# Kernel optimization log

Hardware: AMD Instinct MI355X
Metric: run time of the kernel (lower is better)

Reference implementation:

```python
import jax, jax.numpy as jnp
import numpy as np

B, L, D = 8, 1024, 768          # batch, seq_len, d_model
DI, DS, NL, DC = 1536, 16, 2, 4  # d_inner=2*d_model, d_state, n_layers, d_conv
DECAY, INSCALE = 0.9, 0.1
LN_EPS = 1e-5


def setup_inputs() -> dict:
    key = jax.random.key(0)
    ks = jax.random.split(key, 8)
    return {
        "x": jax.random.normal(ks[0], (B, L, D), jnp.float32),
        "in_proj_w": jax.random.normal(ks[1], (NL, D, 2 * DI), jnp.float32) * 0.02,
        "conv_w": jax.random.normal(ks[2], (NL, DI, DC), jnp.float32) * 0.1,
        "conv_b": jnp.zeros((NL, DI), jnp.float32),
        "out_proj_w": jax.random.normal(ks[3], (NL, DI, D), jnp.float32) * 0.02,
        "ln_gamma": jnp.ones((D,), jnp.float32),
        "ln_beta": jnp.zeros((D,), jnp.float32),
        # per-layer, per-timestep random state matrices (torch.randn inside the scan loop)
        "A": jax.random.normal(ks[4], (NL, L, DI, DS), jnp.float32),
        "Bm": jax.random.normal(ks[5], (NL, L, DS, DI), jnp.float32),
    }


def _silu(v):
    return v * jax.nn.sigmoid(v)


def _causal_dwconv(x, w, b):
    # x: [B, L, DI], w: [DI, DC], b: [DI]; torch Conv1d(groups=DI, padding=DC-1)[..., :L]
    xp = jnp.pad(x, ((0, 0), (DC - 1, 0), (0, 0)))
    out = b
    for k in range(DC):  # tiny fixed kernel loop
        out = out + w[:, k] * xp[:, k:k + L, :]
    return out


def _mamba_block(x, Wi, cw, cb, Wo, A_l, B_l):
    xz = jnp.einsum('bld,de->ble', x, Wi)
    x_in, z = jnp.split(xz, 2, axis=-1)          # each [B, L, DI]
    xc = _silu(_causal_dwconv(x_in, cw, cb))
    # selective scan: h_t = 0.9*h_{t-1} + 0.1 * x_t @ A_t ; y_t = h_t @ B_t
    u = INSCALE * jnp.einsum('blc,lcs->bls', xc, A_l)   # [B, L, DS]
    def step(h, u_t):
        h = DECAY * h + u_t
        return h, h
    _, hs = jax.lax.scan(step, jnp.zeros((x.shape[0], DS), x.dtype),
                         jnp.swapaxes(u, 0, 1))          # hs: [L, B, DS]
    x_ssm = jnp.einsum('lbs,lsc->blc', hs, B_l)          # [B, L, DI]
    y = x_ssm * _silu(z)
    return jnp.einsum('blc,cd->bld', y, Wo)


def reference(x, in_proj_w, conv_w, conv_b, out_proj_w, ln_gamma, ln_beta, A, Bm):
    for i in range(NL):  # residual fallback path of MambaSSM
        x = x + _mamba_block(x, in_proj_w[i], conv_w[i], conv_b[i],
                             out_proj_w[i], A[i], Bm[i])
    mu = jnp.mean(x, axis=-1, keepdims=True)
    var = jnp.mean(jnp.square(x - mu), axis=-1, keepdims=True)
    return (x - mu) / jnp.sqrt(var + LN_EPS) * ln_gamma + ln_beta
```

## Files before the change

### kernel.cpp

```cpp
#include <hip/hip_runtime.h>
#include <cstddef>
#include <cstdint>

constexpr int B  = 8;
constexpr int L  = 1024;
constexpr int D  = 768;
constexpr int DI = 1536;
constexpr int DS = 16;
constexpr int NL = 2;
constexpr float DECAY   = 0.9f;
constexpr float INSCALE = 0.1f;
constexpr float LN_EPS  = 1e-5f;

typedef __attribute__((ext_vector_type(8))) short bf16x8;
typedef __attribute__((ext_vector_type(4))) float f32x4;

typedef __attribute__((address_space(3))) uint32_t       lds_u32;
typedef const __attribute__((address_space(1))) uint32_t glb_u32;

__device__ __forceinline__ float siluf(float v) { return v / (1.0f + expf(-v)); }

__device__ __forceinline__ short f2bf(float f) {
  uint32_t u = __float_as_uint(f);
  u += 0x7fff + ((u >> 16) & 1);
  return (short)(u >> 16);
}
__device__ __forceinline__ float bf2f(short s) {
  return __uint_as_float(((uint32_t)(uint16_t)s) << 16);
}

__device__ __forceinline__ void load_lds16(const short* g, short* l) {
  __builtin_amdgcn_global_load_lds((glb_u32*)g, (lds_u32*)l, 16, 0, 0);
}

__global__ __launch_bounds__(256) void prep_kernel(const float* __restrict__ x,
                                                   short* __restrict__ xb,
                                                   const float* __restrict__ Wi,
                                                   const float* __restrict__ Wo,
                                                   short* __restrict__ Wt_i,
                                                   short* __restrict__ Wt_o) {
  int bid = blockIdx.x;
  if (bid < 6144) {
    int i = bid * 256 + threadIdx.x;
    float4 v = ((const float4*)x)[i];
    short4 s;
    s.x = f2bf(v.x); s.y = f2bf(v.y); s.z = f2bf(v.z); s.w = f2bf(v.w);
    ((short4*)xb)[i] = s;
    return;
  }
  bid -= 6144;
  __shared__ float t[32][33];
  const int layer = bid / 3456;
  bid %= 3456;
  const float* W; short* Wt; int K, N, bx, by;
  if (bid < 2304) {
    W  = Wi  + (size_t)layer * D * 2 * DI;
    Wt = Wt_i + (size_t)layer * 2 * DI * D;
    K = D; N = 2 * DI; bx = bid % 96; by = bid / 96;
  } else {
    bid -= 2304;
    W  = Wo  + (size_t)layer * DI * D;
    Wt = Wt_o + (size_t)layer * D * DI;
    K = DI; N = D; bx = bid % 24; by = bid / 24;
  }
  const int n0 = bx * 32, k0 = by * 32;
  const int tx = threadIdx.x & 31, ty = threadIdx.x >> 5;
#pragma unroll
  for (int r = ty; r < 32; r += 8) t[r][tx] = W[(size_t)(k0 + r) * N + n0 + tx];
  __syncthreads();
#pragma unroll
  for (int r = ty; r < 32; r += 8) Wt[(size_t)(n0 + r) * K + k0 + tx] = f2bf(t[tx][r]);
}

__global__ __launch_bounds__(256) void gemm_bt0(const short* __restrict__ A,
                                                const short* __restrict__ Bt,
                                                short* __restrict__ Pb,
                                                int M, int N, int K) {
  __shared__ short As[3][128 * 32];
  __shared__ short Bs[3][128 * 32];
  const int tid  = threadIdx.x;
  const int lane = tid & 63;
  const int w    = tid >> 6;
  const int wm   = w >> 1;
  const int wn   = w & 1;
  const int bm   = blockIdx.y * 128;
  const int bn   = blockIdx.x * 128;

  const int seg0 = w * 2;
  const int lane16 = lane << 4;
  const int P0 = (seg0 << 10) + lane16;
  const int Q0 = P0 ^ (((P0 >> 7) & 3) << 4);
  const int row0 = Q0 >> 6;
  const int g0   = (Q0 >> 4) & 3;
  const int P1 = ((seg0 + 1) << 10) + lane16;
  const int Q1 = P1 ^ (((P1 >> 7) & 3) << 4);
  const int row1 = Q1 >> 6;
  const int g1   = (Q1 >> 4) & 3;

  const short* gA0 = A  + (size_t)(bm + row0) * K + g0 * 8;
  const short* gA1 = A  + (size_t)(bm + row1) * K + g1 * 8;
  const short* gB0 = Bt + (size_t)(bn + row0) * K + g0 * 8;
  const short* gB1 = Bt + (size_t)(bn + row1) * K + g1 * 8;

  f32x4 acc[4][4];
#pragma unroll
  for (int i = 0; i < 4; ++i)
#pragma unroll
    for (int j = 0; j < 4; ++j) acc[i][j] = (f32x4)(0.f);

  const int fr = lane & 15;
  const int h8 = (lane >> 4) << 3;
  const int NT = K / 32;

  auto stage = [&](int bi, int k0) {
    load_lds16(gA0 + k0, &As[bi][(size_t)seg0 * 512]);
    load_lds16(gA1 + k0, &As[bi][(size_t)(seg0 + 1) * 512]);
    load_lds16(gB0 + k0, &Bs[bi][(size_t)seg0 * 512]);
    load_lds16(gB1 + k0, &Bs[bi][(size_t)(seg0 + 1) * 512]);
  };
  auto compute = [&](int bi) {
    bf16x8 af[4], bfr[4];
#pragma unroll
    for (int i = 0; i < 4; ++i) {
      const int r = wm * 64 + i * 16 + fr;
      int si = (r << 5) + h8;
      si ^= ((r >> 1) & 3) << 3;
      af[i] = *(const bf16x8*)&As[bi][si];
    }
#pragma unroll
    for (int j = 0; j < 4; ++j) {
      const int r = wn * 64 + j * 16 + fr;
      int si = (r << 5) + h8;
      si ^= ((r >> 1) & 3) << 3;
      bfr[j] = *(const bf16x8*)&Bs[bi][si];
    }
#pragma unroll
    for (int i = 0; i < 4; ++i)
#pragma unroll
      for (int j = 0; j < 4; ++j)
        acc[i][j] = __builtin_amdgcn_mfma_f32_16x16x32_bf16(af[i], bfr[j], acc[i][j], 0, 0, 0);
  };

  stage(0, 0);
  stage(1, 32);
  asm volatile("s_waitcnt vmcnt(4)" ::: "memory");
  asm volatile("s_barrier" ::: "memory");

  for (int t = 0; t < NT; t += 3) {
#pragma unroll
    for (int q = 0; q < 3; ++q) {
      const int tt = t + q;
      if (tt + 2 < NT) stage((q + 2) % 3, (tt + 2) * 32);
      compute(q);
      if (tt + 1 < NT) {
        if (tt + 2 < NT) asm volatile("s_waitcnt vmcnt(4)" ::: "memory");
        else             asm volatile("s_waitcnt vmcnt(0)" ::: "memory");
        asm volatile("s_barrier" ::: "memory");
      }
    }
  }

  const int orow = (lane >> 4) * 4;
  const int ocol = lane & 15;
#pragma unroll
  for (int i = 0; i < 4; ++i) {
#pragma unroll
    for (int r = 0; r < 4; ++r) {
      const size_t row = (size_t)(bm + wm * 64 + i * 16 + orow + r);
#pragma unroll
      for (int j = 0; j < 4; ++j) {
        const int col = bn + wn * 64 + j * 16 + ocol;
        float v = acc[i][j][r];
        if (col < DI) Pb[row * DI + col] = f2bf(v);
        else          Pb[(size_t)M * DI + row * DI + col - DI] = f2bf(v);
      }
    }
  }
}

__global__ __launch_bounds__(256) void gemm_bt1(const short* __restrict__ A,
                                                const short* __restrict__ Bt,
                                                short* __restrict__ Pb,
                                                int M, int N, int K) {
  __shared__ short As[4][64 * 32];
  __shared__ short Bs[4][128 * 32];
  const int lane = threadIdx.x & 63;
  const int w    = threadIdx.x >> 6;
  const int bm   = blockIdx.y * 64;
  const int bn   = blockIdx.x * 128;

  const int lane16 = lane << 4;
  const int PA = (w << 10) + lane16;
  const int QA = PA ^ (((PA >> 7) & 3) << 4);
  const int rowA = QA >> 6;
  const int gA_  = (QA >> 4) & 3;
  const int PB0 = ((2 * w) << 10) + lane16;
  const int QB0 = PB0 ^ (((PB0 >> 7) & 3) << 4);
  const int rowB0 = QB0 >> 6;
  const int gB0_  = (QB0 >> 4) & 3;
  const int PB1 = ((2 * w + 1) << 10) + lane16;
  const int QB1 = PB1 ^ (((PB1 >> 7) & 3) << 4);
  const int rowB1 = QB1 >> 6;
  const int gB1_  = (QB1 >> 4) & 3;

  const short* gA  = A  + (size_t)(bm + rowA) * K + gA_ * 8;
  const short* gB0 = Bt + (size_t)(bn + rowB0) * K + gB0_ * 8;
  const short* gB1 = Bt + (size_t)(bn + rowB1) * K + gB1_ * 8;

  f32x4 acc[4][2];
#pragma unroll
  for (int i = 0; i < 4; ++i)
#pragma unroll
    for (int j = 0; j < 2; ++j) acc[i][j] = (f32x4)(0.f);

  const int fr = lane & 15;
  const int h8 = (lane >> 4) << 3;
  const int NT = K / 32;

  auto stage = [&](int bi, int k0) {
    load_lds16(gA  + k0, &As[bi][(size_t)w * 512]);
    load_lds16(gB0 + k0, &Bs[bi][(size_t)(2 * w) * 512]);
    load_lds16(gB1 + k0, &Bs[bi][(size_t)(2 * w + 1) * 512]);
  };
  auto compute = [&](int bi) {
    bf16x8 af[4], bfr[2];
#pragma unroll
    for (int i = 0; i < 4; ++i) {
      const int r = i * 16 + fr;
      int si = (r << 5) + h8;
      si ^= ((r >> 1) & 3) << 3;
      af[i] = *(const bf16x8*)&As[bi][si];
    }
#pragma unroll
    for (int j = 0; j < 2; ++j) {
      const int r = w * 32 + j * 16 + fr;
      int si = (r << 5) + h8;
      si ^= ((r >> 1) & 3) << 3;
      bfr[j] = *(const bf16x8*)&Bs[bi][si];
    }
#pragma unroll
    for (int i = 0; i < 4; ++i)
#pragma unroll
      for (int j = 0; j < 2; ++j)
        acc[i][j] = __builtin_amdgcn_mfma_f32_16x16x32_bf16(af[i], bfr[j], acc[i][j], 0, 0, 0);
  };

  stage(0, 0);
  stage(1, 32);
  stage(2, 64);

  for (int t = 0; t < NT; t += 4) {
#pragma unroll
    for (int q = 0; q < 4; ++q) {
      const int tt = t + q;
      if (tt + 2 < NT)      asm volatile("s_waitcnt vmcnt(6)" ::: "memory");
      else if (tt + 1 < NT) asm volatile("s_waitcnt vmcnt(3)" ::: "memory");
      else                  asm volatile("s_waitcnt vmcnt(0)" ::: "memory");
      asm volatile("s_barrier" ::: "memory");
      if (tt + 3 < NT) stage((tt + 3) & 3, (tt + 3) * 32);
      compute(q);
    }
  }

  const int orow = (lane >> 4) * 4;
  const int ocol = lane & 15;
#pragma unroll
  for (int i = 0; i < 4; ++i) {
#pragma unroll
    for (int r = 0; r < 4; ++r) {
      const size_t row = (size_t)(bm + i * 16 + orow + r);
#pragma unroll
      for (int j = 0; j < 2; ++j) {
        const int col = bn + w * 32 + j * 16 + ocol;
        float o = bf2f(Pb[row * N + col]) + acc[i][j][r];
        Pb[row * N + col] = f2bf(o);
      }
    }
  }
}

constexpr int CSL = DI / 4;
__global__ __launch_bounds__(256) void conv_u_kernel(const short* __restrict__ xin,
                                                     const float* __restrict__ cw,
                                                     const float* __restrict__ cb,
                                                     const float* __restrict__ A_l,
                                                     float* __restrict__ u_part) {
  const int l = blockIdx.x;
  const int p = blockIdx.y;
  const int c_base = p * CSL;
  __shared__ float xs[B][CSL];
  __shared__ float part[4][4][32];

  for (int i = threadIdx.x; i < B * (CSL / 4); i += 256) {
    const int b  = i / (CSL / 4);
    const int c4 = (i % (CSL / 4)) * 4;
    const int c  = c_base + c4;
    float4 q0 = *(const float4*)&cw[(c + 0) * 4];
    float4 q1 = *(const float4*)&cw[(c + 1) * 4];
    float4 q2 = *(const float4*)&cw[(c + 2) * 4];
    float4 q3 = *(const float4*)&cw[(c + 3) * 4];
    float4 acc = *(const float4*)&cb[c];
    const short* xp = xin + (size_t)b * L * DI + c;
#pragma unroll
    for (int k = 0; k < 4; ++k) {
      int lk = l - 3 + k;
      if (lk >= 0) {
        short4 xv = *(const short4*)&xp[(size_t)lk * DI];
        acc.x += (&q0.x)[k] * bf2f(xv.x);
        acc.y += (&q1.x)[k] * bf2f(xv.y);
        acc.z += (&q2.x)[k] * bf2f(xv.z);
        acc.w += (&q3.x)[k] * bf2f(xv.w);
      }
    }
    acc.x = siluf(acc.x); acc.y = siluf(acc.y);
    acc.z = siluf(acc.z); acc.w = siluf(acc.w);
    *(float4*)&xs[b][c4] = acc;
  }
  __syncthreads();

  const int s4 = threadIdx.x & 3;
  const int cg = threadIdx.x >> 2;
  const float* Ap = A_l + (size_t)l * DI * DS + s4 * 4;

  float4 acc[B];
#pragma unroll
  for (int b = 0; b < B; ++b) acc[b] = make_float4(0.f, 0.f, 0.f, 0.f);

#pragma unroll
  for (int c0 = 0; c0 < CSL; c0 += 64) {
    const int cl = c0 + cg;
    float4 a4 = *(const float4*)&Ap[(size_t)(c_base + cl) * DS];
#pragma unroll
    for (int b = 0; b < B; ++b) {
      float xv = xs[b][cl];
      acc[b].x += xv * a4.x; acc[b].y += xv * a4.y;
      acc[b].z += xv * a4.z; acc[b].w += xv * a4.w;
    }
  }

#pragma unroll
  for (int off = 32; off >= 4; off >>= 1) {
#pragma unroll
    for (int b = 0; b < B; ++b) {
      acc[b].x += __shfl_down(acc[b].x, off, 64);
      acc[b].y += __shfl_down(acc[b].y, off, 64);
      acc[b].z += __shfl_down(acc[b].z, off, 64);
      acc[b].w += __shfl_down(acc[b].w, off, 64);
    }
  }
  const int wv = threadIdx.x >> 6, lane = threadIdx.x & 63;
  if (lane < 4) {
#pragma unroll
    for (int b = 0; b < B; ++b) {
      part[wv][lane][b * 4 + 0] = acc[b].x;
      part[wv][lane][b * 4 + 1] = acc[b].y;
      part[wv][lane][b * 4 + 2] = acc[b].z;
      part[wv][lane][b * 4 + 3] = acc[b].w;
    }
  }
  __syncthreads();
  if (threadIdx.x < 128) {
    const int o  = threadIdx.x;
    const int b  = o >> 4;
    const int ss = (o >> 2) & 3;
    const int jj = o & 3;
    float s = part[0][ss][b * 4 + jj] + part[1][ss][b * 4 + jj] +
              part[2][ss][b * 4 + jj] + part[3][ss][b * 4 + jj];
    u_part[((size_t)l * 4 + p) * 128 + o] = INSCALE * s;
  }
}

__global__ __launch_bounds__(256) void scan_kernel(const float* __restrict__ u_part,
                                                   float* __restrict__ hs) {
  const int t = blockIdx.x;
  const int i = threadIdx.x;
  __shared__ float csc[256];

  float v[4];
#pragma unroll
  for (int j = 0; j < 4; ++j) {
    const float* up = u_part + ((size_t)(4 * i + j) * 4) * 128 + t;
    v[j] = (up[0] + up[128]) + (up[256] + up[384]);
  }
  const float p0 = v[0];
  const float p1 = p0 * DECAY + v[1];
  const float p2 = p1 * DECAY + v[2];
  const float p3 = p2 * DECAY + v[3];

  csc[i] = p3;
  __syncthreads();
  float f = DECAY * DECAY * DECAY * DECAY;
  for (int d = 1; d < 256; d <<= 1) {
    float add = (i >= d) ? csc[i - d] : 0.f;
    __syncthreads();
    csc[i] += add * f;
    __syncthreads();
    f *= f;
  }
  const float H = (i > 0) ? csc[i - 1] : 0.f;

  const float a1 = DECAY, a2 = DECAY * DECAY, a3 = a2 * DECAY, a4 = a2 * a2;
  float* hp = hs + (size_t)(4 * i) * 128 + t;
  hp[0]   = p0 + H * a1;
  hp[128] = p1 + H * a2;
  hp[256] = p2 + H * a3;
  hp[384] = p3 + H * a4;
}

__global__ __launch_bounds__(256) void xssm_kernel(const float* __restrict__ hs,
                                                   const float* __restrict__ B_l,
                                                   const short* __restrict__ zb,
                                                   short* __restrict__ y) {
  const int l0 = blockIdx.x * 2;
  const int cb = blockIdx.y * (DI / 3);
  __shared__ float hsl[2][128];
  const int t = threadIdx.x;
  hsl[t >> 7][t & 127] = hs[(size_t)(l0 + (t >> 7)) * 128 + (t & 127)];
  __syncthreads();

  const int li = t >> 7;
  const int l  = l0 + li;
  const int c  = cb + (t & 127) * 4;
  const float* Bp = B_l + (size_t)l * DS * DI + c;

  float4 acc[B];
#pragma unroll
  for (int b = 0; b < B; ++b) acc[b] = make_float4(0.f, 0.f, 0.f, 0.f);
#pragma unroll
  for (int s = 0; s < DS; ++s) {
    float4 bv = *(const float4*)&Bp[(size_t)s * DI];
#pragma unroll
    for (int b = 0; b < B; ++b) {
      float hv = hsl[li][b * DS + s];
      acc[b].x += hv * bv.x; acc[b].y += hv * bv.y;
      acc[b].z += hv * bv.z; acc[b].w += hv * bv.w;
    }
  }
#pragma unroll
  for (int b = 0; b < B; ++b) {
    short4 zs = *(const short4*)&zb[((size_t)b * L + l) * DI + c];
    short4 o;
    o.x = f2bf(acc[b].x * siluf(bf2f(zs.x)));
    o.y = f2bf(acc[b].y * siluf(bf2f(zs.y)));
    o.z = f2bf(acc[b].z * siluf(bf2f(zs.z)));
    o.w = f2bf(acc[b].w * siluf(bf2f(zs.w)));
    *(short4*)&y[((size_t)b * L + l) * DI + c] = o;
  }
}

__global__ __launch_bounds__(256) void ln_kernel(const short* __restrict__ x,
                                                 const float* __restrict__ gam,
                                                 const float* __restrict__ bet,
                                                 float* __restrict__ out) {
  const int row = blockIdx.x;
  const int t = threadIdx.x;
  const short* xr = x + (size_t)row * D;
  float v0 = bf2f(xr[t]), v1 = bf2f(xr[t + 256]), v2 = bf2f(xr[t + 512]);
  float s = v0 + v1 + v2;
  __shared__ float red[4], red2[4];
  const int wid = t >> 6, lane = t & 63;
#pragma unroll
  for (int off = 32; off > 0; off >>= 1) s += __shfl_down(s, off, 64);
  if (lane == 0) red[wid] = s;
  __syncthreads();
  float mu = (red[0] + red[1] + red[2] + red[3]) * (1.0f / D);
  float d0 = v0 - mu, d1 = v1 - mu, d2 = v2 - mu;
  float q = d0 * d0 + d1 * d1 + d2 * d2;
#pragma unroll
  for (int off = 32; off > 0; off >>= 1) q += __shfl_down(q, off, 64);
  if (lane == 0) red2[wid] = q;
  __syncthreads();
  float var = (red2[0] + red2[1] + red2[2] + red2[3]) * (1.0f / D);
  float rstd = rsqrtf(var + LN_EPS);
  size_t base = (size_t)row * D;
  out[base + t]       = d0 * rstd * gam[t]       + bet[t];
  out[base + t + 256] = d1 * rstd * gam[t + 256] + bet[t + 256];
  out[base + t + 512] = d2 * rstd * gam[t + 512] + bet[t + 512];
}

extern "C" void kernel_launch(void* const* d_in, const int* in_sizes, int n_in,
                              void* d_out, int out_size, void* d_ws, size_t ws_size,
                              hipStream_t stream) {
  (void)in_sizes; (void)n_in; (void)out_size; (void)ws_size;
  const float* x   = (const float*)d_in[0];
  const float* Wi  = (const float*)d_in[1];
  const float* cw  = (const float*)d_in[2];
  const float* cb  = (const float*)d_in[3];
  const float* Wo  = (const float*)d_in[4];
  const float* gam = (const float*)d_in[5];
  const float* bet = (const float*)d_in[6];
  const float* Am  = (const float*)d_in[7];
  const float* Bm  = (const float*)d_in[8];
  float* out = (float*)d_out;

  const size_t MN = (size_t)B * L;

  short* buf_xb = (short*)d_ws;
  short* xin_b  = buf_xb + MN * D;
  short* zb     = xin_b + MN * DI;
  short* y_bf   = zb + MN * DI;
  float* u_part = (float*)(y_bf + MN * DI);
  float* buf_hs = u_part + (size_t)L * 4 * 128;
  short* Wt_i   = (short*)(buf_hs + (size_t)L * 128);
  short* Wt_o   = Wt_i + (size_t)NL * 2 * DI * D;

  prep_kernel<<<6144 + 3456 * NL, 256, 0, stream>>>(x, buf_xb, Wi, Wo, Wt_i, Wt_o);

  for (int layer = 0; layer < NL; ++layer) {
    const float* cw_l = cw + (size_t)layer * DI * 4;
    const float* cb_l = cb + (size_t)layer * DI;
    const float* A_l  = Am + (size_t)layer * L * DI * DS;
    const float* B_l  = Bm + (size_t)layer * L * DS * DI;
    const short* Wti_l = Wt_i + (size_t)layer * 2 * DI * D;
    const short* Wto_l = Wt_o + (size_t)layer * D * DI;

    gemm_bt0<<<dim3(2 * DI / 128, MN / 128), 256, 0, stream>>>(
        buf_xb, Wti_l, xin_b, (int)MN, 2 * DI, D);

    conv_u_kernel<<<dim3(L, 4), 256, 0, stream>>>(xin_b, cw_l, cb_l, A_l, u_part);

    scan_kernel<<<128, 256, 0, stream>>>(u_part, buf_hs);

    xssm_kernel<<<dim3(L / 2, 3), 256, 0, stream>>>(buf_hs, B_l, zb, y_bf);

    gemm_bt1<<<dim3(D / 128, MN / 64), 256, 0, stream>>>(
        y_bf, Wto_l, buf_xb, (int)MN, D, DI);
  }

  ln_kernel<<<(int)MN, 256, 0, stream>>>(buf_xb, gam, bet, out);
}
```

Baseline: 441.3 us.

## Rewrite in-proj GEMM as 256x256 tile, 8-wave ping-pong pipeline

Replaces the 128x128, 4-wave in-projection GEMM with a 256x256 tile kernel using 8 waves, a 64-wide K step and a 128 KB LDS double buffer. Global-to-LDS loads are spread across eight phases with barriers, and s_setprio raises wave priority around the MFMA bursts. The intent is more operand reuse per LDS load, fewer blocks and better overlap of memory with compute. The cost is fewer blocks in flight (12x32) and heavier register pressure from the 8x4 accumulators.

```diff
diff --git a/kernel.cpp b/kernel.cpp
--- a/kernel.cpp
+++ b/kernel.cpp
@@ -72,101 +72,131 @@
   for (int r = ty; r < 32; r += 8) Wt[(size_t)(n0 + r) * K + k0 + tx] = f2bf(t[tx][r]);
 }
 
-__global__ __launch_bounds__(256) void gemm_bt0(const short* __restrict__ A,
-                                                const short* __restrict__ Bt,
-                                                short* __restrict__ Pb,
-                                                int M, int N, int K) {
-  __shared__ short As[3][128 * 32];
-  __shared__ short Bs[3][128 * 32];
+__global__ __launch_bounds__(512, 2) void gemm_bt0_8p(const short* __restrict__ Aop,
+                                                      const short* __restrict__ Bt,
+                                                      short* __restrict__ Pb,
+                                                      int M, int N, int K) {
+  __shared__ short lds[65536];
   const int tid  = threadIdx.x;
   const int lane = tid & 63;
   const int w    = tid >> 6;
-  const int wm   = w >> 1;
-  const int wn   = w & 1;
-  const int bm   = blockIdx.y * 128;
-  const int bn   = blockIdx.x * 128;
-
-  const int seg0 = w * 2;
-  const int lane16 = lane << 4;
-  const int P0 = (seg0 << 10) + lane16;
-  const int Q0 = P0 ^ (((P0 >> 7) & 3) << 4);
-  const int row0 = Q0 >> 6;
-  const int g0   = (Q0 >> 4) & 3;
-  const int P1 = ((seg0 + 1) << 10) + lane16;
-  const int Q1 = P1 ^ (((P1 >> 7) & 3) << 4);
-  const int row1 = Q1 >> 6;
-  const int g1   = (Q1 >> 4) & 3;
-
-  const short* gA0 = A  + (size_t)(bm + row0) * K + g0 * 8;
-  const short* gA1 = A  + (size_t)(bm + row1) * K + g1 * 8;
-  const short* gB0 = Bt + (size_t)(bn + row0) * K + g0 * 8;
-  const short* gB1 = Bt + (size_t)(bn + row1) * K + g1 * 8;
-
-  f32x4 acc[4][4];
-#pragma unroll
-  for (int i = 0; i < 4; ++i)
+  const int wm   = w >> 2;
+  const int wn   = w & 3;
+  const int bm   = blockIdx.y * 256;
+  const int bn   = blockIdx.x * 256;
+
+  int srow[2], skc[2];
+#pragma unroll
+  for (int g = 0; g < 2; ++g) {
+    const int P = g * 8192 + tid * 16;
+    const int Q = P ^ (((P >> 7) & 7) << 4);
+    srow[g] = Q >> 7;
+    skc[g]  = (Q >> 4) & 7;
+  }
+
+  auto stageA = [&](int d, int h, int kt) {
+#pragma unroll
+    for (int g = 0; g < 2; ++g)
+      load_lds16(Aop + (size_t)(bm + h * 128 + srow[g]) * K + kt * 64 + skc[g] * 8,
+                 &lds[(d * 2 + h) * 8192 + g * 4096 + tid * 8]);
+  };
+  auto stageB = [&](int d, int h, int kt) {
+#pragma unroll
+    for (int g = 0; g < 2; ++g)
+      load_lds16(Bt + (size_t)(bn + h * 128 + srow[g]) * K + kt * 64 + skc[g] * 8,
+                 &lds[32768 + (d * 2 + h) * 8192 + g * 4096 + tid * 8]);
+  };
+
+  const int fr   = lane & 15;
+  const int hh16 = (lane >> 4) << 4;
+
+  auto rdA = [&](int d, int i, int ks) {
+    const int r  = wm * 128 + i * 16 + fr;
+    const int h  = r >> 7;
+    const int rl = r & 127;
+    int by = rl * 128 + ks * 64 + hh16;
+    by ^= (rl & 7) << 4;
+    return *(const bf16x8*)&lds[(d * 2 + h) * 8192 + (by >> 1)];
+  };
+  auto rdB = [&](int d, int j, int ks) {
+    const int r  = wn * 64 + j * 16 + fr;
+    const int h  = r >> 7;
+    const int rl = r & 127;
+    int by = rl * 128 + ks * 64 + hh16;
+    by ^= (rl & 7) << 4;
+    return *(const bf16x8*)&lds[32768 + (d * 2 + h) * 8192 + (by >> 1)];
+  };
+
+  f32x4 acc[8][4];
+#pragma unroll
+  for (int i = 0; i < 8; ++i)
 #pragma unroll
     for (int j = 0; j < 4; ++j) acc[i][j] = (f32x4)(0.f);
 
-  const int fr = lane & 15;
-  const int h8 = (lane >> 4) << 3;
-  const int NT = K / 32;
-
-  auto stage = [&](int bi, int k0) {
-    load_lds16(gA0 + k0, &As[bi][(size_t)seg0 * 512]);
-    load_lds16(gA1 + k0, &As[bi][(size_t)(seg0 + 1) * 512]);
-    load_lds16(gB0 + k0, &Bs[bi][(size_t)seg0 * 512]);
-    load_lds16(gB1 + k0, &Bs[bi][(size_t)(seg0 + 1) * 512]);
-  };
-  auto compute = [&](int bi) {
-    bf16x8 af[4], bfr[4];
-#pragma unroll
-    for (int i = 0; i < 4; ++i) {
-      const int r = wm * 64 + i * 16 + fr;
-      int si = (r << 5) + h8;
-      si ^= ((r >> 1) & 3) << 3;
-      af[i] = *(const bf16x8*)&As[bi][si];
-    }
-#pragma unroll
-    for (int j = 0; j < 4; ++j) {
-      const int r = wn * 64 + j * 16 + fr;
-      int si = (r << 5) + h8;
-      si ^= ((r >> 1) & 3) << 3;
-      bfr[j] = *(const bf16x8*)&Bs[bi][si];
-    }
-#pragma unroll
-    for (int i = 0; i < 4; ++i)
-#pragma unroll
-      for (int j = 0; j < 4; ++j)
-        acc[i][j] = __builtin_amdgcn_mfma_f32_16x16x32_bf16(af[i], bfr[j], acc[i][j], 0, 0, 0);
-  };
-
-  stage(0, 0);
-  stage(1, 32);
+  const int NTT = K / 64;
+
+  stageB(0, 0, 0); stageB(0, 1, 0);
+  stageA(0, 0, 0); stageA(0, 1, 0);
+  stageB(1, 0, 1); stageB(1, 1, 1);
   asm volatile("s_waitcnt vmcnt(4)" ::: "memory");
   asm volatile("s_barrier" ::: "memory");
 
-  for (int t = 0; t < NT; t += 3) {
-#pragma unroll
-    for (int q = 0; q < 3; ++q) {
-      const int tt = t + q;
-      if (tt + 2 < NT) stage((q + 2) % 3, (tt + 2) * 32);
-      compute(q);
-      if (tt + 1 < NT) {
-        if (tt + 2 < NT) asm volatile("s_waitcnt vmcnt(4)" ::: "memory");
-        else             asm volatile("s_waitcnt vmcnt(0)" ::: "memory");
-        asm volatile("s_barrier" ::: "memory");
+  bf16x8 bfrag[4][2], afrag[2][2];
+
+  for (int t0 = 0; t0 < NTT; t0 += 2) {
+#pragma unroll
+    for (int ph = 0; ph < 8; ++ph) {
+      const int d = ph >> 2;
+      const int q = ph & 3;
+      if (q == 0) {
+#pragma unroll
+        for (int j = 0; j < 4; ++j)
+#pragma unroll
+          for (int ks = 0; ks < 2; ++ks)
+            bfrag[j][ks] = rdB(d, j, ks);
       }
+#pragma unroll
+      for (int ii = 0; ii < 2; ++ii)
+#pragma unroll
+        for (int ks = 0; ks < 2; ++ks)
+          afrag[ii][ks] = rdA(d, q * 2 + ii, ks);
+      switch (ph) {
+        case 0: stageA(1, 0, t0 + 1); break;
+        case 1: stageA(1, 1, t0 + 1); break;
+        case 2: if (t0 + 2 < NTT) stageB(0, 0, t0 + 2); break;
+        case 3: if (t0 + 2 < NTT) stageB(0, 1, t0 + 2); break;
+        case 4: if (t0 + 2 < NTT) stageA(0, 0, t0 + 2); break;
+        case 5: if (t0 + 2 < NTT) stageA(0, 1, t0 + 2); break;
+        case 6: if (t0 + 3 < NTT) stageB(1, 0, t0 + 3); break;
+        case 7: if (t0 + 3 < NTT) stageB(1, 1, t0 + 3); break;
+      }
+      asm volatile("s_barrier" ::: "memory");
+      __builtin_amdgcn_s_setprio(1);
+#pragma unroll
+      for (int ks = 0; ks < 2; ++ks)
+#pragma unroll
+        for (int ii = 0; ii < 2; ++ii)
+#pragma unroll
+          for (int j = 0; j < 4; ++j)
+            acc[q * 2 + ii][j] = __builtin_amdgcn_mfma_f32_16x16x32_bf16(
+                afrag[ii][ks], bfrag[j][ks], acc[q * 2 + ii][j], 0, 0, 0);
+      __builtin_amdgcn_s_setprio(0);
+      if (q == 3) {
+        const bool more = (d == 0) ? (t0 + 2 < NTT) : (t0 + 3 < NTT);
+        if (more) asm volatile("s_waitcnt vmcnt(4)" ::: "memory");
+        else      asm volatile("s_waitcnt vmcnt(0)" ::: "memory");
+      }
+      asm volatile("s_barrier" ::: "memory");
     }
   }
 
   const int orow = (lane >> 4) * 4;
   const int ocol = lane & 15;
 #pragma unroll
-  for (int i = 0; i < 4; ++i) {
+  for (int i = 0; i < 8; ++i) {
 #pragma unroll
     for (int r = 0; r < 4; ++r) {
-      const size_t row = (size_t)(bm + wm * 64 + i * 16 + orow + r);
+      const size_t row = (size_t)(bm + wm * 128 + i * 16 + orow + r);
 #pragma unroll
       for (int j = 0; j < 4; ++j) {
         const int col = bn + wn * 64 + j * 16 + ocol;
@@ -514,7 +544,7 @@
     const short* Wti_l = Wt_i + (size_t)layer * 2 * DI * D;
     const short* Wto_l = Wt_o + (size_t)layer * D * DI;
 
-    gemm_bt0<<<dim3(2 * DI / 128, MN / 128), 256, 0, stream>>>(
+    gemm_bt0_8p<<<dim3(2 * DI / 256, MN / 256), 512, 0, stream>>>(
         buf_xb, Wti_l, xin_b, (int)MN, 2 * DI, D);
 
     conv_u_kernel<<<dim3(L, 4), 256, 0, stream>>>(xin_b, cw_l, cb_l, A_l, u_part);
```

Result: no change. 440.7 us (-0.1%).
